# Optimization experiments

Hardware: AMD Instinct MI355X
Metric: run time of the kernel (lower is better)

The kernel has to match this reference:

```python
import jax, jax.numpy as jnp
import numpy as np

POS_THR = 0.5      # ROI_POSITIVE_THR
NEG_THR = 0.1      # ROI_NEGATIVE_THR
N_SAMPLES = 256    # ROI_SAMPLES
FG_RATIO = 0.25    # ROI_SAMPLE_RATIO
L1W = 1.0          # RPN.L1WEIGHT_INTERSECTION
NUM_FG = int(N_SAMPLES * FG_RATIO)


def _make_boxes(kxy, kwh, shape):
    # valid [x1,y1,x2,y2] boxes in an ~800px image
    xy = jax.random.uniform(kxy, shape[:-1] + (2,)) * 800.0
    wh = jax.random.uniform(kwh, shape[:-1] + (2,)) * 200.0 + 1.0
    return jnp.concatenate([xy, xy + wh], axis=-1)


def setup_inputs() -> dict:
    key = jax.random.key(0)
    k1, k2, k3, k4 = jax.random.split(key, 4)
    proposals = _make_boxes(k1, k2, (16, 16384, 4))  # [B, N, 4]
    gt_boxes = _make_boxes(k3, k4, (16, 128, 4))     # [B, G, 4]
    return {"proposals": proposals, "gt_boxes": gt_boxes}


def _centrehw(b):
    # [x1,y1,x2,y2] -> [cx,cy,w,h]
    x1, y1, x2, y2 = b[..., 0], b[..., 1], b[..., 2], b[..., 3]
    return jnp.stack([(x1 + x2) * 0.5, (y1 + y2) * 0.5, x2 - x1, y2 - y1], axis=-1)


def _targets(gt_c, roi_c):
    dx = (gt_c[..., 0] - roi_c[..., 0]) / roi_c[..., 2]
    dy = (gt_c[..., 1] - roi_c[..., 1]) / roi_c[..., 3]
    dw = jnp.log(gt_c[..., 2] / roi_c[..., 2])
    dh = jnp.log(gt_c[..., 3] / roi_c[..., 3])
    return jnp.stack([dx, dy, dw, dh], axis=-1)


def _iou(prop, gt):
    # prop [B,N,4], gt [B,G,4] -> IoU [B,N,G]
    p = prop[:, :, None, :]
    g = gt[:, None, :, :]
    ix1 = jnp.maximum(p[..., 0], g[..., 0])
    iy1 = jnp.maximum(p[..., 1], g[..., 1])
    ix2 = jnp.minimum(p[..., 2], g[..., 2])
    iy2 = jnp.minimum(p[..., 3], g[..., 3])
    inter = jnp.clip(ix2 - ix1, 0.0) * jnp.clip(iy2 - iy1, 0.0)
    ap = (p[..., 2] - p[..., 0]) * (p[..., 3] - p[..., 1])
    ag = (g[..., 2] - g[..., 0]) * (g[..., 3] - g[..., 1])
    return inter / jnp.maximum(ap + ag - inter, 1e-8)


def _forward(proposals, gt_boxes):
    B, N, _ = proposals.shape
    iou = _iou(proposals, gt_boxes)                       # [B,N,G]
    max_iou = iou.max(axis=-1)                            # [B,N]
    argmax_gt = iou.argmax(axis=-1).astype(jnp.int32)     # [B,N]
    # classify: 1=fg, 0=bg, -1=ignore
    labels = jnp.where(max_iou >= POS_THR, 1,
                       jnp.where(max_iou < NEG_THR, 0, -1)).astype(jnp.int32)
    # randsample: keep <= NUM_FG positives (random), fill rest with negatives.
    r = jax.random.uniform(jax.random.key(1), (B, N))
    pos = labels == 1
    r_pos = jnp.where(pos, r, -1.0)
    order = jnp.argsort(-r_pos, axis=1)
    ranks = jnp.argsort(order, axis=1)                    # rank among positives by r
    pos_sel = pos & (ranks < NUM_FG)
    prio = jnp.where(pos_sel, 3.0 + r,
                     jnp.where(labels == 0, 2.0 + r,
                               jnp.where(pos, 1.0 + r, r)))
    _, idx = jax.lax.top_k(prio, N_SAMPLES)               # [B,S] sampled proposal ids
    batch_labels = jnp.maximum(jnp.take_along_axis(labels, idx, axis=1), 0)  # [B,S]
    roi_batch = jnp.take_along_axis(proposals, idx[..., None], axis=1)       # [B,S,4]
    sel_gt = jnp.take_along_axis(argmax_gt, idx, axis=1)                     # [B,S]
    gt_batch = jnp.take_along_axis(gt_boxes, sel_gt[..., None], axis=1)      # [B,S,4]
    bbox_targets = _targets(_centrehw(gt_batch), _centrehw(roi_batch))       # [B,S,4]
    in_w = jnp.where((batch_labels == 1)[..., None], L1W, 0.0)
    in_w = jnp.broadcast_to(in_w, bbox_targets.shape)
    out_w = (in_w > 0).astype(jnp.float32)
    return roi_batch, batch_labels, bbox_targets, in_w, out_w


def reference(proposals, gt_boxes):
    return _forward(proposals, gt_boxes)
```

## Files before the change

### kernel.cpp

```cpp
#include <hip/hip_runtime.h>
#include <stdint.h>

#define BATCH 16
#define NPROP 16384
#define NGT   128
#define NSAMP 256
#define NFG   64
#define GCAP  512
#define PCAP  8192
#define HCAP  2048
#define NBLK  64
#define BPB   256
#define LOGB  8
#define NEGT  0x780002u

typedef unsigned long long ull;

__device__ __forceinline__ void thr_block(uint32_t c0, uint32_t c1,
                                          uint32_t* o0, uint32_t* o1) {
    const uint32_t k0 = 0u, k1 = 1u, ks2 = 0x1BD11BDBu;
    uint32_t x0 = c0 + k0, x1 = c1 + k1;
#define RND(d) { x0 += x1; x1 = (x1 << d) | (x1 >> (32 - d)); x1 ^= x0; }
    RND(13) RND(15) RND(26) RND(6)   x0 += k1;  x1 += ks2 + 1u;
    RND(17) RND(29) RND(16) RND(24)  x0 += ks2; x1 += k0 + 2u;
    RND(13) RND(15) RND(26) RND(6)   x0 += k0;  x1 += k1 + 3u;
    RND(17) RND(29) RND(16) RND(24)  x0 += k1;  x1 += ks2 + 4u;
    RND(13) RND(15) RND(26) RND(6)   x0 += ks2; x1 += k0 + 5u;
#undef RND
    *o0 = x0; *o1 = x1;
}

__device__ __forceinline__ uint32_t thr_part_xor(uint32_t f) {
    uint32_t a, b; thr_block(0u, f, &a, &b);
    return a ^ b;
}

__global__ void __launch_bounds__(256) k_compute(
    const float* __restrict__ props, const float* __restrict__ gts,
    ull* __restrict__ lists, uint32_t* __restrict__ cntblk)
{
#pragma clang fp contract(off)
    const int b = blockIdx.y;
    const int blk = blockIdx.x;
    const int tid = threadIdx.x;
    const int n = blk * BPB + tid;
    __shared__ float4 g4[NGT];
    __shared__ uint32_t wc[4][4], we_s[4][4];
    if (tid < NGT)
        g4[tid] = ((const float4*)gts)[(size_t)b * NGT + tid];
    __syncthreads();
    const float4 pb = ((const float4*)props)[(size_t)b * NPROP + n];
    const float ap = (pb.z - pb.x) * (pb.w - pb.y);
    float best = -1.0f; int bg = 0;
    #pragma unroll 4
    for (int i = 0; i < NGT; ++i) {
        const float4 gb = g4[i];
        float ag = (gb.z - gb.x) * (gb.w - gb.y);
        float w  = fmaxf(fminf(pb.z, gb.z) - fmaxf(pb.x, gb.x), 0.0f);
        float hh = fmaxf(fminf(pb.w, gb.w) - fmaxf(pb.y, gb.y), 0.0f);
        float inter = w * hh;
        float un = fmaxf(ap + ag - inter, 1e-8f);
        float iou = inter / un;
        if (iou > best) { best = iou; bg = i; }
    }
    uint32_t lab = (best >= 0.5f) ? 2u : ((best < 0.1f) ? 1u : 0u);
    const uint32_t f = (uint32_t)b * NPROP + (uint32_t)n;
    uint32_t mant = thr_part_xor(f) >> 9;
    ull entry = ((ull)(lab == 2u) << 44) | ((ull)mant << 21)
              | ((ull)(16383u - (uint32_t)n) << 7) | (ull)(uint32_t)bg;

    bool cP = (lab == 2u);
    bool cH = (lab == 1u) && (mant >= NEGT);
    bool cL = (lab == 1u) && (mant <  NEGT);
    bool cI = (lab == 0u);
    ull mP = __ballot(cP), mH = __ballot(cH), mL = __ballot(cL), mI = __ballot(cI);
    const int w = tid >> 6;
    const uint32_t lane = (uint32_t)tid & 63u;
    if (lane == 0) {
        wc[0][w] = (uint32_t)__popcll(mP);
        wc[1][w] = (uint32_t)__popcll(mH);
        wc[2][w] = (uint32_t)__popcll(mL);
        wc[3][w] = (uint32_t)__popcll(mI);
    }
    __syncthreads();
    if (tid < 4) {
        uint32_t e = 0;
        #pragma unroll
        for (int i = 0; i < 4; i++) { we_s[tid][i] = e; e += wc[tid][i]; }
        cntblk[((size_t)b * NBLK + blk) * 4 + tid] = e;
    }
    __syncthreads();
    ull lt = lane ? (~0ull >> (64u - lane)) : 0ull;
    ull* slab = lists + (size_t)b * 4 * NPROP;
    const uint32_t segB = (uint32_t)blk * BPB;
    if (cP) slab[0 * NPROP + segB + we_s[0][w] + (uint32_t)__popcll(mP & lt)] = entry;
    if (cH) slab[1 * NPROP + segB + we_s[1][w] + (uint32_t)__popcll(mH & lt)] = entry;
    if (cL) slab[2 * NPROP + segB + we_s[2][w] + (uint32_t)__popcll(mL & lt)] = entry;
    if (cI) slab[3 * NPROP + segB + we_s[3][w] + (uint32_t)__popcll(mI & lt)] = entry;
}

__global__ void __launch_bounds__(1024) k_select(
    const float* __restrict__ props, const float* __restrict__ gts,
    const ull* __restrict__ lists, const uint32_t* __restrict__ cntblk,
    float* __restrict__ out)
{
#pragma clang fp contract(off)
    const int b = blockIdx.x;
    const int tid = threadIdx.x;
    const int wid = tid >> 6;
    const uint32_t lane = (uint32_t)tid & 63u;
    __shared__ ull      dpos[PCAP];
    __shared__ ull      dnh[HCAP];
    __shared__ uint32_t hist[2048];
    __shared__ ull      gat[GCAP];
    __shared__ ull      selk[NSAMP];
    __shared__ uint32_t sela[NSAMP];
    __shared__ uint32_t bc[NBLK * 4];
    __shared__ uint32_t tot[4];
    __shared__ uint32_t sh_dig, sh_k, sh_cnt_in, gcnt, selc, stP, stH;
    __shared__ ull sh_thr;

    const ull* Spos = lists + ((size_t)b * 4 + 0) * NPROP;
    const ull* SnH  = lists + ((size_t)b * 4 + 1) * NPROP;
    const ull* SnL  = lists + ((size_t)b * 4 + 2) * NPROP;
    const ull* Sign = lists + ((size_t)b * 4 + 3) * NPROP;
    if (tid == 0) { selc = 0; stP = 0; stH = 0; }
    if (tid < NBLK * 4) bc[tid] = cntblk[(size_t)b * NBLK * 4 + tid];
    __syncthreads();
    if (tid < 4) {
        uint32_t run = 0;
        for (int blk = 0; blk < NBLK; ++blk) run += bc[blk * 4 + tid];
        tot[tid] = run;
    }
    __syncthreads();
    const uint32_t npos = tot[0], nH = tot[1], nL = tot[2], nig = tot[3];
    const uint32_t nneg = nH + nL;
    const uint32_t npn  = npos + nneg;
    const bool dP = (npos <= PCAP), dH = (nH <= HCAP);

    for (int s4 = 0; s4 < 4; ++s4) {
        uint32_t seg = (uint32_t)(wid * 4 + s4);
        if (dP) {
            uint32_t c = bc[seg * 4 + 0];
            for (uint32_t i0 = 0; i0 < c; i0 += 64) {
                uint32_t take = (c - i0 < 64u) ? (c - i0) : 64u;
                uint32_t s0 = 0;
                if (lane == 0) s0 = atomicAdd(&stP, take);
                s0 = (uint32_t)__shfl((int)s0, 0);
                if (lane < take) dpos[s0 + lane] = Spos[seg * BPB + i0 + lane];
            }
        }
        if (dH) {
            uint32_t c = bc[seg * 4 + 1];
            for (uint32_t i0 = 0; i0 < c; i0 += 64) {
                uint32_t take = (c - i0 < 64u) ? (c - i0) : 64u;
                uint32_t s0 = 0;
                if (lane == 0) s0 = atomicAdd(&stH, take);
                s0 = (uint32_t)__shfl((int)s0, 0);
                if (lane < take) dnh[s0 + lane] = SnH[seg * BPB + i0 + lane];
            }
        }
    }
    __syncthreads();

    const uint32_t MSEG = NBLK * BPB;
    const uint32_t mPos = dP ? npos : MSEG;
    const uint32_t mH   = dH ? nH   : MSEG;
    auto posEnt = [&](uint32_t j, bool& e) -> ull {
        if (dP) { e = true; return dpos[j]; }
        e = (j & (BPB - 1u)) < bc[(j >> LOGB) * 4 + 0];
        return e ? Spos[j] : 0ull;
    };
    auto nhEnt = [&](uint32_t j, bool& e) -> ull {
        if (dH) { e = true; return dnh[j]; }
        e = (j & (BPB - 1u)) < bc[(j >> LOGB) * 4 + 1];
        return e ? SnH[j] : 0ull;
    };
    auto nlEnt = [&](uint32_t j, bool& e) -> ull {
        e = (j & (BPB - 1u)) < bc[(j >> LOGB) * 4 + 2];
        return e ? SnL[j] : 0ull;
    };
    auto igEnt = [&](uint32_t j, bool& e) -> ull {
        e = (j & (BPB - 1u)) < bc[(j >> LOGB) * 4 + 3];
        return e ? Sign[j] : 0ull;
    };

    auto keyA_of = [](ull e) -> ull {
        return (((e >> 21) & 0x7FFFFFull) << 14) | ((e >> 7) & 0x3FFFull);
    };

    auto locate = [&](uint32_t k) {
        if (tid < 64) {
            uint32_t cs = 0;
            if (lane < 32) {
                const uint32_t base = lane * 64u;
                #pragma unroll 8
                for (uint32_t i = 0; i < 64; i++)
                    cs += hist[base + ((i + lane) & 63u)];
            }
            uint32_t s = cs;
            #pragma unroll
            for (int off = 1; off < 32; off <<= 1) {
                uint32_t t = __shfl_down(s, off);
                if (lane + off < 32) s += t;
            }
            uint32_t sExcl = s - cs;
            bool cond = (lane < 32) && (sExcl < k) && (k <= s);
            ull ball = __ballot(cond);
            uint32_t cstar = (uint32_t)(__ffsll((unsigned long long)ball) - 1);
            uint32_t kc = (uint32_t)__shfl((int)(k - sExcl), (int)cstar);
            uint32_t val = hist[cstar * 64u + lane];
            uint32_t fi = val;
            #pragma unroll
            for (int off = 1; off < 64; off <<= 1) {
                uint32_t t = __shfl_down(fi, off);
                if (lane + off < 64) fi += t;
            }
            uint32_t fExcl = fi - val;
            bool cond2 = (fExcl < kc) && (kc <= fi);
            ull ball2 = __ballot(cond2);
            uint32_t bstar = (uint32_t)(__ffsll((unsigned long long)ball2) - 1);
            if (lane == bstar) {
                sh_dig = cstar * 64u + lane;
                sh_k = kc - fExcl;
                sh_cnt_in = val;
            }
        }
    };

    auto radix = [&](auto&& kf, uint32_t m, uint32_t k, int shift) -> ull {
        if (m <= GCAP) {
            if (tid == 0) gcnt = 0;
            __syncthreads();
            for (uint32_t j = tid; j < m; j += 1024) {
                bool e; ull key = kf(j, e);
                if (e) { uint32_t s = atomicAdd(&gcnt, 1u); gat[s] = key; }
            }
            __syncthreads();
            uint32_t gc = gcnt;
            if (tid < (int)gc) {
                ull x = gat[tid];
                uint32_t r = 0;
                for (uint32_t j = 0; j < gc; j++) r += (gat[j] > x);
                if (r == k - 1) sh_thr = x;
            }
            __syncthreads();
            return sh_thr;
        }
        ull prefix = 0, mask = 0;
        for (;;) {
            hist[tid] = 0; hist[tid + 1024] = 0;
            __syncthreads();
            for (uint32_t j = tid; j < m; j += 1024) {
                bool e; ull key = kf(j, e);
                if (e && ((key ^ prefix) & mask) == 0)
                    atomicAdd(&hist[(uint32_t)(key >> shift) & 2047u], 1u);
            }
            __syncthreads();
            locate(k);
            __syncthreads();
            uint32_t dig = sh_dig, kk = sh_k, cnt = sh_cnt_in;
            prefix |= ((ull)dig) << shift;
            mask   |= 2047ull << shift;
            if (cnt <= GCAP || shift == 0) {
                if (tid == 0) gcnt = 0;
                __syncthreads();
                for (uint32_t j = tid; j < m; j += 1024) {
                    bool e; ull key = kf(j, e);
                    if (e && ((key ^ prefix) & mask) == 0) {
                        uint32_t s = atomicAdd(&gcnt, 1u);
                        if (s < GCAP) gat[s] = key;
                    }
                }
                __syncthreads();
                uint32_t gc = (gcnt < GCAP) ? gcnt : GCAP;
                if (tid < (int)gc) {
                    ull x = gat[tid];
                    uint32_t r = 0;
                    for (uint32_t j = 0; j < gc; j++) r += (gat[j] > x);
                    if (r == kk - 1) sh_thr = x;
                }
                __syncthreads();
                return sh_thr;
            } else {
                k = kk;
                shift = (shift >= 11) ? shift - 11 : 0;
                __syncthreads();
            }
        }
    };

    ull thrA = 0;
    if (npos > NFG) {
        thrA = radix([&](uint32_t j, bool& e) -> ull {
            ull ent = posEnt(j, e); return keyA_of(ent); }, mPos, NFG, 26);
    }

    auto keyB_pos = [&](ull ent) -> ull {
        uint32_t mant = (uint32_t)((ent >> 21) & 0x7FFFFFull);
        uint32_t invn = (uint32_t)((ent >> 7) & 0x3FFFull);
        float r = __uint_as_float(0x3F800000u | mant) - 1.0f;
        uint32_t cls = (keyA_of(ent) >= thrA) ? 3u : 1u;
        float prio = (float)cls + r;
        return (((ull)__float_as_uint(prio)) << 14) | (ull)invn;
    };
    auto keyB_neg = [](ull ent) -> ull {
        uint32_t mant = (uint32_t)((ent >> 21) & 0x7FFFFFull);
        uint32_t invn = (uint32_t)((ent >> 7) & 0x3FFFull);
        float r = __uint_as_float(0x3F800000u | mant) - 1.0f;
        float prio = 2.0f + r;
        return (((ull)__float_as_uint(prio)) << 14) | (ull)invn;
    };
    auto keyB_ign = [](ull ent) -> ull {
        uint32_t mant = (uint32_t)((ent >> 21) & 0x7FFFFFull);
        uint32_t invn = (uint32_t)((ent >> 7) & 0x3FFFull);
        float r = __uint_as_float(0x3F800000u | mant) - 1.0f;
        float prio = 0.0f + r;
        return (((ull)__float_as_uint(prio)) << 14) | (ull)invn;
    };

    const uint32_t c3 = (npos < NFG) ? npos : NFG;
    const uint32_t c2 = nneg;
    uint32_t clsStar = (npn >= NSAMP) ? ((NSAMP <= c3 + c2) ? 2u : 1u) : 0u;
    bool scanL = true;
    const bool scanI = (clsStar == 0u);
    ull thrB = 0;
    if (clsStar == 2u) {
        uint32_t k2 = NSAMP - c3;
        if (nH >= k2) {
            scanL = false;
            thrB = radix([&](uint32_t j, bool& e) -> ull {
                ull ent = nhEnt(j, e); return keyB_neg(ent); }, mH, k2, 26);
        } else {
            thrB = radix([&](uint32_t j, bool& e) -> ull {
                if (j < mH) { ull ent = nhEnt(j, e); return keyB_neg(ent); }
                ull ent = nlEnt(j - mH, e); return keyB_neg(ent); },
                mH + MSEG, k2, 26);
        }
    } else if (clsStar == 1u) {
        thrB = radix([&](uint32_t j, bool& e) -> ull {
            ull ent = posEnt(j, e);
            ull kb = keyB_pos(ent);
            e = e && ((kb >> 14) < 0x40000000ull);
            return kb; }, mPos, NSAMP - c3 - c2, 26);
    } else {
        thrB = radix([&](uint32_t j, bool& e) -> ull {
            ull ent = igEnt(j, e); return keyB_ign(ent); }, MSEG, NSAMP - npn, 34);
    }
    __syncthreads();

    auto push = [&](ull key, ull ent, uint32_t fg) {
        uint32_t s = atomicAdd(&selc, 1u);
        if (s < NSAMP) { selk[s] = key; sela[s] = (fg << 7) | (uint32_t)(ent & 0x7Full); }
    };
    for (uint32_t j = tid; j < mPos; j += 1024) {
        bool e; ull ent = posEnt(j, e);
        if (!e) continue;
        ull key = keyB_pos(ent);
        if (clsStar == 0u || key >= thrB) push(key, ent, 1u);
    }
    for (uint32_t j = tid; j < mH; j += 1024) {
        bool e; ull ent = nhEnt(j, e);
        if (!e) continue;
        ull key = keyB_neg(ent);
        if (clsStar == 0u || key >= thrB) push(key, ent, 0u);
    }
    if (scanL) {
        for (uint32_t j = tid; j < MSEG; j += 1024) {
            bool e; ull ent = nlEnt(j, e);
            if (!e) continue;
            ull key = keyB_neg(ent);
            if (clsStar == 0u || key >= thrB) push(key, ent, 0u);
        }
    }
    if (scanI) {
        for (uint32_t j = tid; j < MSEG; j += 1024) {
            bool e; ull ent = igEnt(j, e);
            if (!e) continue;
            ull key = keyB_ign(ent);
            if (key >= thrB) push(key, ent, 0u);
        }
    }
    __syncthreads();

    if (tid < NSAMP) {
        ull x = selk[tid];
        uint32_t r = 0;
        for (int j = 0; j < NSAMP; j++) r += (selk[j] > x);
        uint32_t n = 16383u - (uint32_t)(x & 0x3FFFull);
        uint32_t aux = sela[tid];
        uint32_t bg = aux & 0x7Fu;
        const int isfg = (int)((aux >> 7) & 1u);
        const float4 pb = ((const float4*)props)[(size_t)b * NPROP + n];
        const float4 gb = ((const float4*)gts)[(size_t)b * NGT + bg];
        const size_t O_ROI = 0;
        const size_t O_LBL = (size_t)BATCH * NSAMP * 4;
        const size_t O_TGT = O_LBL + (size_t)BATCH * NSAMP;
        const size_t O_INW = O_TGT + (size_t)BATCH * NSAMP * 4;
        const size_t O_OUW = O_INW + (size_t)BATCH * NSAMP * 4;
        const size_t row = (size_t)b * NSAMP + r;
        out[O_ROI + row * 4 + 0] = pb.x;
        out[O_ROI + row * 4 + 1] = pb.y;
        out[O_ROI + row * 4 + 2] = pb.z;
        out[O_ROI + row * 4 + 3] = pb.w;
        out[O_LBL + row] = isfg ? 1.0f : 0.0f;
        float rw  = pb.z - pb.x, rh = pb.w - pb.y;
        float gw  = gb.z - gb.x, gh = gb.w - gb.y;
        out[O_TGT + row * 4 + 0] = ((gb.x + gb.z) * 0.5f - (pb.x + pb.z) * 0.5f) / rw;
        out[O_TGT + row * 4 + 1] = ((gb.y + gb.w) * 0.5f - (pb.y + pb.w) * 0.5f) / rh;
        out[O_TGT + row * 4 + 2] = logf(gw / rw);
        out[O_TGT + row * 4 + 3] = logf(gh / rh);
        float wv = isfg ? 1.0f : 0.0f;
        for (int c = 0; c < 4; c++) {
            out[O_INW + row * 4 + c] = wv;
            out[O_OUW + row * 4 + c] = wv;
        }
    }
}

extern "C" void kernel_launch(void* const* d_in, const int* in_sizes, int n_in,
                              void* d_out, int out_size, void* d_ws, size_t ws_size,
                              hipStream_t stream) {
    (void)in_sizes; (void)n_in; (void)out_size; (void)ws_size;
    const float* props = (const float*)d_in[0];
    const float* gts   = (const float*)d_in[1];
    ull* lists = (ull*)d_ws;
    uint32_t* cntblk = (uint32_t*)((char*)d_ws + (size_t)BATCH * 4 * NPROP * 8);
    float* out = (float*)d_out;

    dim3 gridA(NBLK, BATCH);
    k_compute<<<gridA, 256, 0, stream>>>(props, gts, lists, cntblk);
    k_select<<<BATCH, 1024, 0, stream>>>(props, gts, lists, cntblk, out);
}
```

Before: 102.5 us.

## Merge negative lists and fuse histogram building into the shared-memory staging pass

```diff
diff --git a/kernel.cpp b/kernel.cpp
--- a/kernel.cpp
+++ b/kernel.cpp
@@ -8,11 +8,10 @@
 #define NFG   64
 #define GCAP  512
 #define PCAP  8192
-#define HCAP  2048
+#define HCAP  4096
 #define NBLK  64
 #define BPB   256
 #define LOGB  8
-#define NEGT  0x780002u
 
 typedef unsigned long long ull;
 
@@ -45,7 +44,7 @@
     const int tid = threadIdx.x;
     const int n = blk * BPB + tid;
     __shared__ float4 g4[NGT];
-    __shared__ uint32_t wc[4][4], we_s[4][4];
+    __shared__ uint32_t wc[3][4], we_s[3][4];
     if (tid < NGT)
         g4[tid] = ((const float4*)gts)[(size_t)b * NGT + tid];
     __syncthreads();
@@ -70,20 +69,18 @@
               | ((ull)(16383u - (uint32_t)n) << 7) | (ull)(uint32_t)bg;
 
     bool cP = (lab == 2u);
-    bool cH = (lab == 1u) && (mant >= NEGT);
-    bool cL = (lab == 1u) && (mant <  NEGT);
+    bool cN = (lab == 1u);
     bool cI = (lab == 0u);
-    ull mP = __ballot(cP), mH = __ballot(cH), mL = __ballot(cL), mI = __ballot(cI);
+    ull mP = __ballot(cP), mN = __ballot(cN), mI = __ballot(cI);
     const int w = tid >> 6;
     const uint32_t lane = (uint32_t)tid & 63u;
     if (lane == 0) {
         wc[0][w] = (uint32_t)__popcll(mP);
-        wc[1][w] = (uint32_t)__popcll(mH);
-        wc[2][w] = (uint32_t)__popcll(mL);
-        wc[3][w] = (uint32_t)__popcll(mI);
-    }
-    __syncthreads();
-    if (tid < 4) {
+        wc[1][w] = (uint32_t)__popcll(mN);
+        wc[2][w] = (uint32_t)__popcll(mI);
+    }
+    __syncthreads();
+    if (tid < 3) {
         uint32_t e = 0;
         #pragma unroll
         for (int i = 0; i < 4; i++) { we_s[tid][i] = e; e += wc[tid][i]; }
@@ -94,9 +91,8 @@
     ull* slab = lists + (size_t)b * 4 * NPROP;
     const uint32_t segB = (uint32_t)blk * BPB;
     if (cP) slab[0 * NPROP + segB + we_s[0][w] + (uint32_t)__popcll(mP & lt)] = entry;
-    if (cH) slab[1 * NPROP + segB + we_s[1][w] + (uint32_t)__popcll(mH & lt)] = entry;
-    if (cL) slab[2 * NPROP + segB + we_s[2][w] + (uint32_t)__popcll(mL & lt)] = entry;
-    if (cI) slab[3 * NPROP + segB + we_s[3][w] + (uint32_t)__popcll(mI & lt)] = entry;
+    if (cN) slab[1 * NPROP + segB + we_s[1][w] + (uint32_t)__popcll(mN & lt)] = entry;
+    if (cI) slab[2 * NPROP + segB + we_s[2][w] + (uint32_t)__popcll(mI & lt)] = entry;
 }
 
 __global__ void __launch_bounds__(1024) k_select(
@@ -110,192 +106,66 @@
     const int wid = tid >> 6;
     const uint32_t lane = (uint32_t)tid & 63u;
     __shared__ ull      dpos[PCAP];
-    __shared__ ull      dnh[HCAP];
-    __shared__ uint32_t hist[2048];
-    __shared__ ull      gat[GCAP];
+    __shared__ ull      dneg[HCAP];
+    __shared__ uint32_t histA[2048];
+    __shared__ uint32_t histB[2048];
+    __shared__ ull      gatA[GCAP];
+    __shared__ ull      gatB[GCAP];
     __shared__ ull      selk[NSAMP];
     __shared__ uint32_t sela[NSAMP];
     __shared__ uint32_t bc[NBLK * 4];
-    __shared__ uint32_t tot[4];
-    __shared__ uint32_t sh_dig, sh_k, sh_cnt_in, gcnt, selc, stP, stH;
-    __shared__ ull sh_thr;
+    __shared__ uint32_t preP[NBLK], preN[NBLK], tot[3];
+    __shared__ uint32_t shA[3], shB[3], shS[3];
+    __shared__ uint32_t gcA, gcB, gcnt, selc;
+    __shared__ ull sh_thrA, sh_thrB, sh_thr;
 
     const ull* Spos = lists + ((size_t)b * 4 + 0) * NPROP;
-    const ull* SnH  = lists + ((size_t)b * 4 + 1) * NPROP;
-    const ull* SnL  = lists + ((size_t)b * 4 + 2) * NPROP;
-    const ull* Sign = lists + ((size_t)b * 4 + 3) * NPROP;
-    if (tid == 0) { selc = 0; stP = 0; stH = 0; }
+    const ull* Sneg = lists + ((size_t)b * 4 + 1) * NPROP;
+    const ull* Sign = lists + ((size_t)b * 4 + 2) * NPROP;
+
     if (tid < NBLK * 4) bc[tid] = cntblk[(size_t)b * NBLK * 4 + tid];
-    __syncthreads();
-    if (tid < 4) {
-        uint32_t run = 0;
-        for (int blk = 0; blk < NBLK; ++blk) run += bc[blk * 4 + tid];
-        tot[tid] = run;
-    }
-    __syncthreads();
-    const uint32_t npos = tot[0], nH = tot[1], nL = tot[2], nig = tot[3];
-    const uint32_t nneg = nH + nL;
+    histA[tid] = 0; histA[tid + 1024] = 0;
+    histB[tid] = 0; histB[tid + 1024] = 0;
+    if (tid == 0) { gcA = 0; gcB = 0; gcnt = 0; selc = 0; }
+    __syncthreads();
+    if (wid < 3) {
+        uint32_t own = bc[lane * 4 + (uint32_t)wid];
+        uint32_t v = own;
+        #pragma unroll
+        for (int off = 1; off < 64; off <<= 1) {
+            uint32_t t = (uint32_t)__shfl_up((int)v, off);
+            if (lane >= (uint32_t)off) v += t;
+        }
+        if (wid == 0) preP[lane] = v - own;
+        else if (wid == 1) preN[lane] = v - own;
+        if (lane == 63) tot[wid] = v;
+    }
+    __syncthreads();
+    const uint32_t npos = tot[0], nneg = tot[1], nig = tot[2];
     const uint32_t npn  = npos + nneg;
-    const bool dP = (npos <= PCAP), dH = (nH <= HCAP);
-
-    for (int s4 = 0; s4 < 4; ++s4) {
-        uint32_t seg = (uint32_t)(wid * 4 + s4);
-        if (dP) {
-            uint32_t c = bc[seg * 4 + 0];
-            for (uint32_t i0 = 0; i0 < c; i0 += 64) {
-                uint32_t take = (c - i0 < 64u) ? (c - i0) : 64u;
-                uint32_t s0 = 0;
-                if (lane == 0) s0 = atomicAdd(&stP, take);
-                s0 = (uint32_t)__shfl((int)s0, 0);
-                if (lane < take) dpos[s0 + lane] = Spos[seg * BPB + i0 + lane];
-            }
-        }
-        if (dH) {
-            uint32_t c = bc[seg * 4 + 1];
-            for (uint32_t i0 = 0; i0 < c; i0 += 64) {
-                uint32_t take = (c - i0 < 64u) ? (c - i0) : 64u;
-                uint32_t s0 = 0;
-                if (lane == 0) s0 = atomicAdd(&stH, take);
-                s0 = (uint32_t)__shfl((int)s0, 0);
-                if (lane < take) dnh[s0 + lane] = SnH[seg * BPB + i0 + lane];
-            }
-        }
-    }
-    __syncthreads();
-
-    const uint32_t MSEG = NBLK * BPB;
-    const uint32_t mPos = dP ? npos : MSEG;
-    const uint32_t mH   = dH ? nH   : MSEG;
-    auto posEnt = [&](uint32_t j, bool& e) -> ull {
-        if (dP) { e = true; return dpos[j]; }
-        e = (j & (BPB - 1u)) < bc[(j >> LOGB) * 4 + 0];
-        return e ? Spos[j] : 0ull;
-    };
-    auto nhEnt = [&](uint32_t j, bool& e) -> ull {
-        if (dH) { e = true; return dnh[j]; }
-        e = (j & (BPB - 1u)) < bc[(j >> LOGB) * 4 + 1];
-        return e ? SnH[j] : 0ull;
-    };
-    auto nlEnt = [&](uint32_t j, bool& e) -> ull {
-        e = (j & (BPB - 1u)) < bc[(j >> LOGB) * 4 + 2];
-        return e ? SnL[j] : 0ull;
-    };
-    auto igEnt = [&](uint32_t j, bool& e) -> ull {
-        e = (j & (BPB - 1u)) < bc[(j >> LOGB) * 4 + 3];
-        return e ? Sign[j] : 0ull;
-    };
+    const uint32_t c3   = (npos < NFG) ? npos : NFG;
+    const uint32_t k2   = NSAMP - c3;
+    const bool dP = (npos <= PCAP), dH = (nneg <= HCAP);
+    const bool fast0 = (npn >= NSAMP) && (c3 + nneg >= NSAMP) && dP && dH;
 
     auto keyA_of = [](ull e) -> ull {
         return (((e >> 21) & 0x7FFFFFull) << 14) | ((e >> 7) & 0x3FFFull);
     };
-
-    auto locate = [&](uint32_t k) {
-        if (tid < 64) {
-            uint32_t cs = 0;
-            if (lane < 32) {
-                const uint32_t base = lane * 64u;
-                #pragma unroll 8
-                for (uint32_t i = 0; i < 64; i++)
-                    cs += hist[base + ((i + lane) & 63u)];
-            }
-            uint32_t s = cs;
-            #pragma unroll
-            for (int off = 1; off < 32; off <<= 1) {
-                uint32_t t = __shfl_down(s, off);
-                if (lane + off < 32) s += t;
-            }
-            uint32_t sExcl = s - cs;
-            bool cond = (lane < 32) && (sExcl < k) && (k <= s);
-            ull ball = __ballot(cond);
-            uint32_t cstar = (uint32_t)(__ffsll((unsigned long long)ball) - 1);
-            uint32_t kc = (uint32_t)__shfl((int)(k - sExcl), (int)cstar);
-            uint32_t val = hist[cstar * 64u + lane];
-            uint32_t fi = val;
-            #pragma unroll
-            for (int off = 1; off < 64; off <<= 1) {
-                uint32_t t = __shfl_down(fi, off);
-                if (lane + off < 64) fi += t;
-            }
-            uint32_t fExcl = fi - val;
-            bool cond2 = (fExcl < kc) && (kc <= fi);
-            ull ball2 = __ballot(cond2);
-            uint32_t bstar = (uint32_t)(__ffsll((unsigned long long)ball2) - 1);
-            if (lane == bstar) {
-                sh_dig = cstar * 64u + lane;
-                sh_k = kc - fExcl;
-                sh_cnt_in = val;
-            }
-        }
-    };
-
-    auto radix = [&](auto&& kf, uint32_t m, uint32_t k, int shift) -> ull {
-        if (m <= GCAP) {
-            if (tid == 0) gcnt = 0;
-            __syncthreads();
-            for (uint32_t j = tid; j < m; j += 1024) {
-                bool e; ull key = kf(j, e);
-                if (e) { uint32_t s = atomicAdd(&gcnt, 1u); gat[s] = key; }
-            }
-            __syncthreads();
-            uint32_t gc = gcnt;
-            if (tid < (int)gc) {
-                ull x = gat[tid];
-                uint32_t r = 0;
-                for (uint32_t j = 0; j < gc; j++) r += (gat[j] > x);
-                if (r == k - 1) sh_thr = x;
-            }
-            __syncthreads();
-            return sh_thr;
-        }
-        ull prefix = 0, mask = 0;
-        for (;;) {
-            hist[tid] = 0; hist[tid + 1024] = 0;
-            __syncthreads();
-            for (uint32_t j = tid; j < m; j += 1024) {
-                bool e; ull key = kf(j, e);
-                if (e && ((key ^ prefix) & mask) == 0)
-                    atomicAdd(&hist[(uint32_t)(key >> shift) & 2047u], 1u);
-            }
-            __syncthreads();
-            locate(k);
-            __syncthreads();
-            uint32_t dig = sh_dig, kk = sh_k, cnt = sh_cnt_in;
-            prefix |= ((ull)dig) << shift;
-            mask   |= 2047ull << shift;
-            if (cnt <= GCAP || shift == 0) {
-                if (tid == 0) gcnt = 0;
-                __syncthreads();
-                for (uint32_t j = tid; j < m; j += 1024) {
-                    bool e; ull key = kf(j, e);
-                    if (e && ((key ^ prefix) & mask) == 0) {
-                        uint32_t s = atomicAdd(&gcnt, 1u);
-                        if (s < GCAP) gat[s] = key;
-                    }
-                }
-                __syncthreads();
-                uint32_t gc = (gcnt < GCAP) ? gcnt : GCAP;
-                if (tid < (int)gc) {
-                    ull x = gat[tid];
-                    uint32_t r = 0;
-                    for (uint32_t j = 0; j < gc; j++) r += (gat[j] > x);
-                    if (r == kk - 1) sh_thr = x;
-                }
-                __syncthreads();
-                return sh_thr;
-            } else {
-                k = kk;
-                shift = (shift >= 11) ? shift - 11 : 0;
-                __syncthreads();
-            }
-        }
-    };
-
+    auto keyB_neg = [](ull ent) -> ull {
+        uint32_t mant = (uint32_t)((ent >> 21) & 0x7FFFFFull);
+        uint32_t invn = (uint32_t)((ent >> 7) & 0x3FFFull);
+        float r = __uint_as_float(0x3F800000u | mant) - 1.0f;
+        float prio = 2.0f + r;
+        return (((ull)__float_as_uint(prio)) << 14) | (ull)invn;
+    };
+    auto keyB_ign = [](ull ent) -> ull {
+        uint32_t mant = (uint32_t)((ent >> 21) & 0x7FFFFFull);
+        uint32_t invn = (uint32_t)((ent >> 7) & 0x3FFFull);
+        float r = __uint_as_float(0x3F800000u | mant) - 1.0f;
+        float prio = 0.0f + r;
+        return (((ull)__float_as_uint(prio)) << 14) | (ull)invn;
+    };
     ull thrA = 0;
-    if (npos > NFG) {
-        thrA = radix([&](uint32_t j, bool& e) -> ull {
-            ull ent = posEnt(j, e); return keyA_of(ent); }, mPos, NFG, 26);
-    }
-
     auto keyB_pos = [&](ull ent) -> ull {
         uint32_t mant = (uint32_t)((ent >> 21) & 0x7FFFFFull);
         uint32_t invn = (uint32_t)((ent >> 7) & 0x3FFFull);
@@ -304,84 +174,235 @@
         float prio = (float)cls + r;
         return (((ull)__float_as_uint(prio)) << 14) | (ull)invn;
     };
-    auto keyB_neg = [](ull ent) -> ull {
-        uint32_t mant = (uint32_t)((ent >> 21) & 0x7FFFFFull);
-        uint32_t invn = (uint32_t)((ent >> 7) & 0x3FFFull);
-        float r = __uint_as_float(0x3F800000u | mant) - 1.0f;
-        float prio = 2.0f + r;
-        return (((ull)__float_as_uint(prio)) << 14) | (ull)invn;
-    };
-    auto keyB_ign = [](ull ent) -> ull {
-        uint32_t mant = (uint32_t)((ent >> 21) & 0x7FFFFFull);
-        uint32_t invn = (uint32_t)((ent >> 7) & 0x3FFFull);
-        float r = __uint_as_float(0x3F800000u | mant) - 1.0f;
-        float prio = 0.0f + r;
-        return (((ull)__float_as_uint(prio)) << 14) | (ull)invn;
-    };
-
-    const uint32_t c3 = (npos < NFG) ? npos : NFG;
-    const uint32_t c2 = nneg;
-    uint32_t clsStar = (npn >= NSAMP) ? ((NSAMP <= c3 + c2) ? 2u : 1u) : 0u;
-    bool scanL = true;
-    const bool scanI = (clsStar == 0u);
-    ull thrB = 0;
-    if (clsStar == 2u) {
-        uint32_t k2 = NSAMP - c3;
-        if (nH >= k2) {
-            scanL = false;
-            thrB = radix([&](uint32_t j, bool& e) -> ull {
-                ull ent = nhEnt(j, e); return keyB_neg(ent); }, mH, k2, 26);
-        } else {
-            thrB = radix([&](uint32_t j, bool& e) -> ull {
-                if (j < mH) { ull ent = nhEnt(j, e); return keyB_neg(ent); }
-                ull ent = nlEnt(j - mH, e); return keyB_neg(ent); },
-                mH + MSEG, k2, 26);
-        }
-    } else if (clsStar == 1u) {
-        thrB = radix([&](uint32_t j, bool& e) -> ull {
-            ull ent = posEnt(j, e);
-            ull kb = keyB_pos(ent);
-            e = e && ((kb >> 14) < 0x40000000ull);
-            return kb; }, mPos, NSAMP - c3 - c2, 26);
-    } else {
-        thrB = radix([&](uint32_t j, bool& e) -> ull {
-            ull ent = igEnt(j, e); return keyB_ign(ent); }, MSEG, NSAMP - npn, 34);
-    }
-    __syncthreads();
-
     auto push = [&](ull key, ull ent, uint32_t fg) {
         uint32_t s = atomicAdd(&selc, 1u);
         if (s < NSAMP) { selk[s] = key; sela[s] = (fg << 7) | (uint32_t)(ent & 0x7Full); }
     };
-    for (uint32_t j = tid; j < mPos; j += 1024) {
-        bool e; ull ent = posEnt(j, e);
-        if (!e) continue;
-        ull key = keyB_pos(ent);
-        if (clsStar == 0u || key >= thrB) push(key, ent, 1u);
-    }
-    for (uint32_t j = tid; j < mH; j += 1024) {
-        bool e; ull ent = nhEnt(j, e);
-        if (!e) continue;
-        ull key = keyB_neg(ent);
-        if (clsStar == 0u || key >= thrB) push(key, ent, 0u);
-    }
-    if (scanL) {
-        for (uint32_t j = tid; j < MSEG; j += 1024) {
-            bool e; ull ent = nlEnt(j, e);
+
+    for (int s4 = 0; s4 < 4; ++s4) {
+        uint32_t seg = (uint32_t)(wid * 4 + s4);
+        if (dP) {
+            uint32_t c = bc[seg * 4 + 0], bb = preP[seg];
+            for (uint32_t i = lane; i < c; i += 64) {
+                ull ent = Spos[seg * BPB + i];
+                dpos[bb + i] = ent;
+                if (fast0 && npos > NFG)
+                    atomicAdd(&histA[(uint32_t)(keyA_of(ent) >> 26) & 2047u], 1u);
+            }
+        }
+        if (dH) {
+            uint32_t c = bc[seg * 4 + 1], bb = preN[seg];
+            for (uint32_t i = lane; i < c; i += 64) {
+                ull ent = Sneg[seg * BPB + i];
+                dneg[bb + i] = ent;
+                if (fast0)
+                    atomicAdd(&histB[(uint32_t)(keyB_neg(ent) >> 26) & 2047u], 1u);
+            }
+        }
+    }
+    __syncthreads();
+
+    auto locW = [&](const uint32_t* h, uint32_t k, uint32_t* o3) {
+        uint32_t cs = 0;
+        if (lane < 32) {
+            const uint32_t base = lane * 64u;
+            #pragma unroll 8
+            for (uint32_t i = 0; i < 64; i++) cs += h[base + ((i + lane) & 63u)];
+        }
+        uint32_t s = cs;
+        #pragma unroll
+        for (int off = 1; off < 32; off <<= 1) {
+            uint32_t t = __shfl_down(s, off);
+            if (lane + off < 32) s += t;
+        }
+        uint32_t sExcl = s - cs;
+        bool cond = (lane < 32) && (sExcl < k) && (k <= s);
+        ull ball = __ballot(cond);
+        uint32_t cstar = (uint32_t)(__ffsll((unsigned long long)ball) - 1);
+        uint32_t kc_ = (uint32_t)__shfl((int)(k - sExcl), (int)cstar);
+        uint32_t val = h[cstar * 64u + lane];
+        uint32_t fi = val;
+        #pragma unroll
+        for (int off = 1; off < 64; off <<= 1) {
+            uint32_t t = __shfl_down(fi, off);
+            if (lane + off < 64) fi += t;
+        }
+        uint32_t fExcl = fi - val;
+        bool cond2 = (fExcl < kc_) && (kc_ <= fi);
+        ull ball2 = __ballot(cond2);
+        uint32_t bstar = (uint32_t)(__ffsll((unsigned long long)ball2) - 1);
+        if (lane == bstar) { o3[0] = cstar * 64u + lane; o3[1] = kc_ - fExcl; o3[2] = val; }
+    };
+
+    bool fast = fast0;
+    if (fast) {
+        if (wid == 0 && npos > NFG) locW(histA, NFG, shA);
+        if (wid == 1)               locW(histB, k2,  shB);
+        __syncthreads();
+        if ((npos > NFG && shA[2] > GCAP) || (shB[2] > GCAP)) fast = false;
+    }
+    if (fast) {
+        if (npos > NFG) {
+            uint32_t digA = shA[0];
+            for (uint32_t j = tid; j < npos; j += 1024) {
+                ull k = keyA_of(dpos[j]);
+                if (((uint32_t)(k >> 26) & 2047u) == digA) gatA[atomicAdd(&gcA, 1u)] = k;
+            }
+        }
+        {
+            uint32_t digB = shB[0];
+            for (uint32_t j = tid; j < nneg; j += 1024) {
+                ull k = keyB_neg(dneg[j]);
+                if (((uint32_t)(k >> 26) & 2047u) == digB) gatB[atomicAdd(&gcB, 1u)] = k;
+            }
+        }
+        __syncthreads();
+        if (npos > NFG) {
+            if ((uint32_t)tid < gcA) {
+                ull x = gatA[tid]; uint32_t r = 0;
+                for (uint32_t j = 0; j < gcA; j++) r += (gatA[j] > x);
+                if (r == shA[1] - 1) sh_thrA = x;
+            }
+        } else if (tid == 0) sh_thrA = 0;
+        if (tid >= 512 && (uint32_t)(tid - 512) < gcB) {
+            ull x = gatB[tid - 512]; uint32_t r = 0;
+            for (uint32_t j = 0; j < gcB; j++) r += (gatB[j] > x);
+            if (r == shB[1] - 1) sh_thrB = x;
+        }
+        __syncthreads();
+        thrA = sh_thrA;
+        const ull thrB = sh_thrB;
+        for (uint32_t j = tid; j < npos; j += 1024) {
+            ull ent = dpos[j];
+            if (keyA_of(ent) >= thrA) push(keyB_pos(ent), ent, 1u);
+        }
+        for (uint32_t j = tid; j < nneg; j += 1024) {
+            ull ent = dneg[j];
+            ull k = keyB_neg(ent);
+            if (k >= thrB) push(k, ent, 0u);
+        }
+        __syncthreads();
+    }
+    if (!fast) {
+        const uint32_t MSEG = NBLK * BPB;
+        const uint32_t mPos = dP ? npos : MSEG;
+        const uint32_t mNeg = dH ? nneg : MSEG;
+        auto posEnt = [&](uint32_t j, bool& e) -> ull {
+            if (dP) { e = true; return dpos[j]; }
+            e = (j & (BPB - 1u)) < bc[(j >> LOGB) * 4 + 0];
+            return e ? Spos[j] : 0ull;
+        };
+        auto negEnt = [&](uint32_t j, bool& e) -> ull {
+            if (dH) { e = true; return dneg[j]; }
+            e = (j & (BPB - 1u)) < bc[(j >> LOGB) * 4 + 1];
+            return e ? Sneg[j] : 0ull;
+        };
+        auto igEnt = [&](uint32_t j, bool& e) -> ull {
+            e = (j & (BPB - 1u)) < bc[(j >> LOGB) * 4 + 2];
+            return e ? Sign[j] : 0ull;
+        };
+        auto radix = [&](auto&& kf, uint32_t m, uint32_t k, int shift) -> ull {
+            if (m <= GCAP) {
+                if (tid == 0) gcnt = 0;
+                __syncthreads();
+                for (uint32_t j = tid; j < m; j += 1024) {
+                    bool e; ull key = kf(j, e);
+                    if (e) { uint32_t s = atomicAdd(&gcnt, 1u); gatA[s] = key; }
+                }
+                __syncthreads();
+                uint32_t gc = gcnt;
+                if ((uint32_t)tid < gc) {
+                    ull x = gatA[tid]; uint32_t r = 0;
+                    for (uint32_t j = 0; j < gc; j++) r += (gatA[j] > x);
+                    if (r == k - 1) sh_thr = x;
+                }
+                __syncthreads();
+                return sh_thr;
+            }
+            ull prefix = 0, mask = 0;
+            for (;;) {
+                histA[tid] = 0; histA[tid + 1024] = 0;
+                __syncthreads();
+                for (uint32_t j = tid; j < m; j += 1024) {
+                    bool e; ull key = kf(j, e);
+                    if (e && ((key ^ prefix) & mask) == 0)
+                        atomicAdd(&histA[(uint32_t)(key >> shift) & 2047u], 1u);
+                }
+                __syncthreads();
+                if (tid < 64) locW(histA, k, shS);
+                __syncthreads();
+                uint32_t dig = shS[0], kk = shS[1], cnt = shS[2];
+                prefix |= ((ull)dig) << shift;
+                mask   |= 2047ull << shift;
+                if (cnt <= GCAP || shift == 0) {
+                    if (tid == 0) gcnt = 0;
+                    __syncthreads();
+                    for (uint32_t j = tid; j < m; j += 1024) {
+                        bool e; ull key = kf(j, e);
+                        if (e && ((key ^ prefix) & mask) == 0) {
+                            uint32_t s = atomicAdd(&gcnt, 1u);
+                            if (s < GCAP) gatA[s] = key;
+                        }
+                    }
+                    __syncthreads();
+                    uint32_t gc = (gcnt < GCAP) ? gcnt : GCAP;
+                    if ((uint32_t)tid < gc) {
+                        ull x = gatA[tid]; uint32_t r = 0;
+                        for (uint32_t j = 0; j < gc; j++) r += (gatA[j] > x);
+                        if (r == kk - 1) sh_thr = x;
+                    }
+                    __syncthreads();
+                    return sh_thr;
+                } else {
+                    k = kk;
+                    shift = (shift >= 11) ? shift - 11 : 0;
+                    __syncthreads();
+                }
+            }
+        };
+
+        if (npos > NFG) {
+            thrA = radix([&](uint32_t j, bool& e) -> ull {
+                ull ent = posEnt(j, e); return keyA_of(ent); }, mPos, NFG, 26);
+        }
+        uint32_t clsStar = (npn >= NSAMP) ? ((NSAMP <= c3 + nneg) ? 2u : 1u) : 0u;
+        ull thrB = 0;
+        if (clsStar == 2u) {
+            thrB = radix([&](uint32_t j, bool& e) -> ull {
+                ull ent = negEnt(j, e); return keyB_neg(ent); }, mNeg, k2, 26);
+        } else if (clsStar == 1u) {
+            thrB = radix([&](uint32_t j, bool& e) -> ull {
+                ull ent = posEnt(j, e);
+                ull kb = keyB_pos(ent);
+                e = e && ((kb >> 14) < 0x40000000ull);
+                return kb; }, mPos, NSAMP - c3 - nneg, 26);
+        } else {
+            thrB = radix([&](uint32_t j, bool& e) -> ull {
+                ull ent = igEnt(j, e); return keyB_ign(ent); }, MSEG, NSAMP - npn, 34);
+        }
+        __syncthreads();
+        for (uint32_t j = tid; j < mPos; j += 1024) {
+            bool e; ull ent = posEnt(j, e);
+            if (!e) continue;
+            ull key = keyB_pos(ent);
+            if (clsStar == 0u || key >= thrB) push(key, ent, 1u);
+        }
+        for (uint32_t j = tid; j < mNeg; j += 1024) {
+            bool e; ull ent = negEnt(j, e);
             if (!e) continue;
             ull key = keyB_neg(ent);
             if (clsStar == 0u || key >= thrB) push(key, ent, 0u);
         }
-    }
-    if (scanI) {
-        for (uint32_t j = tid; j < MSEG; j += 1024) {
-            bool e; ull ent = igEnt(j, e);
-            if (!e) continue;
-            ull key = keyB_ign(ent);
-            if (key >= thrB) push(key, ent, 0u);
-        }
-    }
-    __syncthreads();
+        if (clsStar == 0u) {
+            for (uint32_t j = tid; j < MSEG; j += 1024) {
+                bool e; ull ent = igEnt(j, e);
+                if (!e) continue;
+                ull key = keyB_ign(ent);
+                if (key >= thrB) push(key, ent, 0u);
+            }
+        }
+        __syncthreads();
+    }
 
     if (tid < NSAMP) {
         ull x = selk[tid];
```

New measurement: 99.08 us. -3.3%, faster.
